# Kernel optimization log

Measured on AMD Instinct MI355X. Metric: run time of the kernel, lower is better.

## Reference

```python
import jax, jax.numpy as jnp
import numpy as np

H_IMG, W_IMG = 64, 64          # token grid (n = H*W = 4096)
D_MODEL = 512
N_HEADS = 8
D1 = 1024                      # expand_ratio * d_model, multiple of n_heads
HEAD_DIM = D1 // N_HEADS       # 128
RANK = 32
NK = 16                        # inducing points for SKI interpolation


def interp_weights(n, nk):
    # inverse-time warp: position i -> 1/(i+1) in (0,1], linearly interpolated
    # onto nk uniform inducing points in [0,1] (2 nonzeros per row).
    pos = 1.0 / (jnp.arange(n, dtype=jnp.float32) + 1.0)
    t = pos * (nk - 1)
    idx = jnp.clip(jnp.floor(t).astype(jnp.int32), 0, nk - 2)
    frac = t - idx.astype(jnp.float32)
    r = jnp.arange(n)
    Wm = jnp.zeros((n, nk), jnp.float32)
    Wm = Wm.at[r, idx].set(1.0 - frac).at[r, idx + 1].set(frac)
    return Wm  # (n, nk)


def apply_toep(v, U, V):
    # v: (b, m, n, h, d); low-rank SKI Toeplitz mixing along axis n.
    # T ~= (Wm @ U) (Wm @ V)^T per head  -> O(n*r*d) instead of O(n^2*d).
    n = v.shape[2]
    nk = U.shape[1]
    Wm = interp_weights(n, nk)                      # (n, nk)
    A = jnp.einsum('nk,hkr->hnr', Wm, U)            # (h, n, r)
    B = jnp.einsum('nk,hkr->hnr', Wm, V)            # (h, n, r)
    tmp = jnp.einsum('hnr,bmnhd->bmhrd', B, v)      # contract over n
    return jnp.einsum('hnr,bmhrd->bmnhd', A, tmp)


def setup_inputs() -> dict:
    key = jax.random.key(0)
    ks = jax.random.split(key, 12)
    s = 0.02
    x = jax.random.normal(ks[0], (16, H_IMG * W_IMG, D_MODEL), jnp.float32)
    Wu = s * jax.random.normal(ks[1], (D1, D_MODEL), jnp.float32)
    bu = s * jax.random.normal(ks[2], (D1,), jnp.float32)
    Wv = s * jax.random.normal(ks[3], (D1, D_MODEL), jnp.float32)
    bv = s * jax.random.normal(ks[4], (D1,), jnp.float32)
    Wo = s * jax.random.normal(ks[5], (D_MODEL, D1), jnp.float32)
    bo = s * jax.random.normal(ks[6], (D_MODEL,), jnp.float32)
    U1 = s * jax.random.normal(ks[7], (N_HEADS, NK, RANK), jnp.float32)
    V1 = s * jax.random.normal(ks[8], (N_HEADS, NK, RANK), jnp.float32)
    U2 = s * jax.random.normal(ks[9], (N_HEADS, NK, RANK), jnp.float32)
    V2 = s * jax.random.normal(ks[10], (N_HEADS, NK, RANK), jnp.float32)
    return {'x': x, 'Wu': Wu, 'bu': bu, 'Wv': Wv, 'bv': bv, 'Wo': Wo,
            'bo': bo, 'U1': U1, 'V1': V1, 'U2': U2, 'V2': V2}


def reference(x, Wu, bu, Wv, bv, Wo, bo, U1, V1, U2, V2):
    b, n, _ = x.shape
    H = int(np.sqrt(n)); W = n // H
    u = jax.nn.silu(x @ Wu.T + bu)                  # (b, n, d1)
    v = jax.nn.silu(x @ Wv.T + bv)                  # (b, n, d1)
    v4 = v.reshape(b, H, W, N_HEADS, HEAD_DIM)      # (b, H, W, h, d)

    # o1: toep1 along W, then toep2 along H
    t = apply_toep(v4, U1, V1)                      # mix along W
    t = t.transpose(0, 2, 1, 3, 4)                  # (b, W, H, h, d)
    t = apply_toep(t, U2, V2)                       # mix along H
    o1 = t.transpose(0, 2, 1, 3, 4)

    # o2: toep2 along H, then toep1 along W
    s_ = v4.transpose(0, 2, 1, 3, 4)                # (b, W, H, h, d)
    s_ = apply_toep(s_, U2, V2)                     # mix along H
    s_ = s_.transpose(0, 2, 1, 3, 4)                # (b, H, W, h, d)
    o2 = apply_toep(s_, U1, V1)                     # mix along W

    out = (o1 + o2).reshape(b, n, D1)
    out = u * out                                   # gated token mixing
    return out @ Wo.T + bo                          # (b, n, d_model)
```

## Files before the change

kernel.cpp:

```cpp
#include <hip/hip_runtime.h>
#include <hip/hip_bf16.h>

typedef unsigned short u16;
typedef unsigned int   u32;
typedef float  f32x4  __attribute__((ext_vector_type(4)));
typedef __bf16 bf16x8 __attribute__((ext_vector_type(8)));
typedef u16    u16x8  __attribute__((ext_vector_type(8)));
typedef u16    u16x4  __attribute__((ext_vector_type(4)));

__device__ __forceinline__ u16 f2bf(float f) {
  u32 x = __builtin_bit_cast(u32, f);
  x += 0x7fffu + ((x >> 16) & 1u);
  return (u16)(x >> 16);
}
__device__ __forceinline__ float bf2f(u16 u) {
  return __builtin_bit_cast(float, (u32)u << 16);
}
__device__ __forceinline__ void gload_lds16(const u16* g, u16* l) {
  __builtin_amdgcn_global_load_lds(
      (const __attribute__((address_space(1))) void*)g,
      (__attribute__((address_space(3))) void*)l, 16, 0, 0);
}

__global__ void k_conv_x(const float* __restrict__ x, u16* __restrict__ xb) {
  int g = blockIdx.x * 256 + threadIdx.x;
  const float4* src = (const float4*)(x + (size_t)g * 8);
  float4 f0 = src[0], f1 = src[1];
  u16x8 o;
  o[0]=f2bf(f0.x); o[1]=f2bf(f0.y); o[2]=f2bf(f0.z); o[3]=f2bf(f0.w);
  o[4]=f2bf(f1.x); o[5]=f2bf(f1.y); o[6]=f2bf(f1.z); o[7]=f2bf(f1.w);
  *(u16x8*)(xb + (size_t)g * 8) = o;
}

__global__ void k_conv_w(const float* __restrict__ Wu, const float* __restrict__ Wv,
                         const float* __restrict__ Wo, const float* __restrict__ bu,
                         const float* __restrict__ bv, u16* __restrict__ wuvb,
                         u16* __restrict__ wob, float* __restrict__ biasuv) {
  int g = blockIdx.x * 256 + threadIdx.x;
  int e = g * 4;
  const float* src; u16* dst;
  if (e < 524288)        { src = Wu + e;             dst = wuvb + e; }
  else if (e < 1048576)  { src = Wv + (e - 524288);  dst = wuvb + e; }
  else                   { src = Wo + (e - 1048576); dst = wob + (e - 1048576); }
  float4 f = *(const float4*)src;
  u16x4 o; o[0]=f2bf(f.x); o[1]=f2bf(f.y); o[2]=f2bf(f.z); o[3]=f2bf(f.w);
  *(u16x4*)dst = o;
  if (g < 2048) biasuv[g] = (g < 1024) ? bu[g] : bv[g - 1024];
}

__global__ void k_toep(const float* __restrict__ U1, const float* __restrict__ V1,
                       const float* __restrict__ U2, const float* __restrict__ V2,
                       u16* __restrict__ T1b, u16* __restrict__ T2b) {
  __shared__ float Us[512], Vs[512];
  int bid = blockIdx.x, t = threadIdx.x;
  int which = bid >> 6, rest = bid & 63, h = rest >> 3, seg = rest & 7;
  const float* U = which ? U2 : U1;
  const float* V = which ? V2 : V1;
  u16* T = which ? T2b : T1b;
  float scale = which ? 2.0f : 1.0f;
  for (int i = t; i < 512; i += 256) { Us[i] = U[h*512 + i]; Vs[i] = V[h*512 + i]; }
  __syncthreads();
  for (int q = 0; q < 2; ++q) {
    int e = seg * 512 + q * 256 + t;
    int i = e >> 6, j = e & 63;
    float pi = 1.0f / (float)(i + 1); float tvi = pi * 15.0f;
    int ii = min((int)floorf(tvi), 14); float fi = tvi - (float)ii;
    float pj = 1.0f / (float)(j + 1); float tvj = pj * 15.0f;
    int jj = min((int)floorf(tvj), 14); float fj = tvj - (float)jj;
    float s = 0.0f;
    #pragma unroll
    for (int r = 0; r < 32; ++r) {
      float a = (1.0f - fi) * Us[ii*32 + r] + fi * Us[(ii+1)*32 + r];
      float b = (1.0f - fj) * Vs[jj*32 + r] + fj * Vs[(jj+1)*32 + r];
      s += a * b;
    }
    T[h*4096 + i*64 + j] = f2bf(s * scale);
  }
}

template<int EPI>
__global__ __launch_bounds__(512, 2) void k_gemm256(
    const u16* __restrict__ A, const u16* __restrict__ B,
    const float* __restrict__ bias, void* __restrict__ C,
    int K, int nbn, int ldc) {
  extern __shared__ uint4 smem4[];
  u16* lds = (u16*)smem4;
  const int t = threadIdx.x;
  const int l = t & 63, w = t >> 6;
  const int wmi = w >> 2, wni = w & 3;
  const int nwg = gridDim.x;
  const int lb = (blockIdx.x & 7) * (nwg >> 3) + (blockIdx.x >> 3);
  const int bm = lb / nbn, bn = lb % nbn;
  const u16* Ab = A + (size_t)bm * 256 * K;
  const u16* Bb = B + (size_t)bn * 256 * K;
  const int NT = K >> 6;

  f32x4 acc[8][4];
  #pragma unroll
  for (int i = 0; i < 8; ++i)
    #pragma unroll
    for (int j = 0; j < 4; ++j) acc[i][j] = (f32x4){0.f, 0.f, 0.f, 0.f};

#define STAGE(gop) do {                                                      \
    int _g = (gop);                                                          \
    int _tile = _g >> 2, _half = _g & 3;                                     \
    int _kt = _tile << 6;                                                    \
    const u16* _src = (_half < 2) ? Ab : Bb;                                 \
    int _rowbase = (_half & 1) << 7;                                         \
    u16* _dst = lds + (_tile & 1) * 32768 + ((_half >= 2) ? 16384 : 0)       \
                + _rowbase * 64;                                             \
    _Pragma("unroll")                                                        \
    for (int _j = 0; _j < 2; ++_j) {                                         \
      int _idx = _j * 512 + t;                                               \
      int _rr = _idx >> 3, _s8 = _idx & 7;                                   \
      int _R = _rowbase + _rr;                                               \
      int _col = (_s8 ^ (_R & 7)) << 3;                                      \
      gload_lds16(_src + (size_t)_R * K + _kt + _col, _dst + _idx * 8);      \
    }                                                                        \
  } while (0)

#define READ_A(hh, fp) do {                                                  \
    _Pragma("unroll")                                                        \
    for (int ks = 0; ks < 2; ++ks)                                           \
      _Pragma("unroll")                                                      \
      for (int i = 0; i < 2; ++i) {                                          \
        int R = ((hh) << 7) + (wmi << 6) + ((fp) * 2 + i) * 16 + (l & 15);   \
        int q8 = ks * 4 + (l >> 4);                                          \
        af[ks*2+i] = *(const bf16x8*)&As[R * 64 + ((q8 ^ (R & 7)) << 3)];    \
      }                                                                      \
  } while (0)

#define MFMA_PHASE(hh, fp) do {                                              \
    __builtin_amdgcn_s_setprio(1);                                           \
    _Pragma("unroll")                                                        \
    for (int ks = 0; ks < 2; ++ks)                                           \
      _Pragma("unroll")                                                      \
      for (int i = 0; i < 2; ++i)                                            \
        _Pragma("unroll")                                                    \
        for (int nf = 0; nf < 4; ++nf)                                       \
          acc[(hh)*4+(fp)*2+i][nf] = __builtin_amdgcn_mfma_f32_16x16x32_bf16(\
              af[ks*2+i], bfv[ks*4+nf], acc[(hh)*4+(fp)*2+i][nf], 0, 0, 0);  \
    __builtin_amdgcn_s_setprio(0);                                           \
  } while (0)

  STAGE(0); STAGE(1); STAGE(2); STAGE(3);
  STAGE(6); STAGE(7); STAGE(4);
  asm volatile("s_waitcnt vmcnt(6)");
  __builtin_amdgcn_s_barrier();

  for (int tile = 0; tile < NT; ++tile) {
    const u16* As = lds + (tile & 1) * 32768;
    const u16* Bs = As + 16384;
    bf16x8 bfv[8];
    bf16x8 af[4];

    #pragma unroll
    for (int ks = 0; ks < 2; ++ks)
      #pragma unroll
      for (int nf = 0; nf < 4; ++nf) {
        int R = (wni << 6) + nf * 16 + (l & 15);
        int q8 = ks * 4 + (l >> 4);
        bfv[ks*4+nf] = *(const bf16x8*)&Bs[R * 64 + ((q8 ^ (R & 7)) << 3)];
      }
    READ_A(0, 0);
    if (tile + 1 < NT) STAGE(4 * (tile + 1) + 1);
    __builtin_amdgcn_s_barrier();
    asm volatile("s_waitcnt lgkmcnt(0)");
    MFMA_PHASE(0, 0);
    __builtin_amdgcn_s_barrier();

    READ_A(0, 1);
    if (tile + 2 < NT) { STAGE(4*(tile+2)+2); STAGE(4*(tile+2)+3); }
    __builtin_amdgcn_s_barrier();
    asm volatile("s_waitcnt lgkmcnt(0)");
    MFMA_PHASE(0, 1);
    if (tile < NT - 2)       asm volatile("s_waitcnt vmcnt(12)");
    else if (tile == NT - 2) asm volatile("s_waitcnt vmcnt(8)");
    else                     asm volatile("s_waitcnt vmcnt(0)");
    __builtin_amdgcn_s_barrier();

    READ_A(1, 0);
    if (tile + 2 < NT) STAGE(4 * (tile + 2) + 0);
    __builtin_amdgcn_s_barrier();
    asm volatile("s_waitcnt lgkmcnt(0)");
    MFMA_PHASE(1, 0);
    __builtin_amdgcn_s_barrier();

    READ_A(1, 1);
    __builtin_amdgcn_s_barrier();
    asm volatile("s_waitcnt lgkmcnt(0)");
    MFMA_PHASE(1, 1);
    if (tile < NT - 2)       asm volatile("s_waitcnt vmcnt(8)");
    else if (tile == NT - 2) asm volatile("s_waitcnt vmcnt(2)");
    __builtin_amdgcn_s_barrier();
  }
#undef STAGE
#undef READ_A
#undef MFMA_PHASE

  float bcol[4];
  #pragma unroll
  for (int nf = 0; nf < 4; ++nf)
    bcol[nf] = bias[bn * 256 + (wni << 6) + nf * 16 + (l & 15)];
  #pragma unroll
  for (int hf = 0; hf < 8; ++hf) {
    int gm0 = bm * 256 + (hf >> 2) * 128 + wmi * 64 + (hf & 3) * 16 + (l >> 4) * 4;
    #pragma unroll
    for (int nf = 0; nf < 4; ++nf) {
      int gn = bn * 256 + (wni << 6) + nf * 16 + (l & 15);
      #pragma unroll
      for (int r = 0; r < 4; ++r) {
        float z = acc[hf][nf][r] + bcol[nf];
        size_t off = (size_t)(gm0 + r) * ldc + gn;
        if (EPI == 0) {
          z = z / (1.0f + __expf(-z));
          ((u16*)C)[off] = f2bf(z);
        } else {
          ((float*)C)[off] = z;
        }
      }
    }
  }
}

template<int PASS>
__global__ __launch_bounds__(256) void k_mix(const u16* __restrict__ uv,
                                             u16* __restrict__ y,
                                             const u16* __restrict__ Tmat) {
  __shared__ alignas(16) u16 Ts[64 * 72];
  __shared__ alignas(16) u32 VT[128 * 36];
  int bid = blockIdx.x, t = threadIdx.x;
  int h = bid & 7, outer = (bid >> 3) & 63, b = bid >> 9;
  int l = t & 63, w = t >> 6;

  {
    const u16* Tg = Tmat + h * 4096;
    int rr = t >> 2, cc = (t & 3) * 16;
    const uint4* src = (const uint4*)(Tg + rr * 64 + cc);
    uint4 v0 = src[0], v1 = src[1];
    *(uint4*)&Ts[rr * 72 + cc] = v0;
    *(uint4*)&Ts[rr * 72 + cc + 8] = v1;
  }

  size_t inbase; size_t instride;
  if (PASS == 0) { inbase = ((size_t)(b*64 + outer) * 64) * 2048 + 1024 + h*128; instride = 2048; }
  else           { inbase = ((size_t)b * 4096 + outer) * 1024 + h*128;            instride = 65536; }
  const u16* inp = (PASS == 0) ? uv : (const u16*)y;

  #pragma unroll
  for (int a2 = 0; a2 < 2; ++a2) {
    int jp = (t >> 4) + a2 * 16;
    int dc = t & 15;
    const u16* r0 = inp + inbase + (size_t)(2*jp) * instride + dc * 8;
    const u16* r1 = r0 + instride;
    uint4 av = *(const uint4*)r0;
    uint4 bv = *(const uint4*)r1;
    u32 a4[4] = {av.x, av.y, av.z, av.w};
    u32 b4[4] = {bv.x, bv.y, bv.z, bv.w};
    #pragma unroll
    for (int ww = 0; ww < 4; ++ww) {
      u32 lo = (a4[ww] & 0xffffu) | (b4[ww] << 16);
      u32 hi = (a4[ww] >> 16) | (b4[ww] & 0xffff0000u);
      int d0 = dc * 8 + 2 * ww, d1 = d0 + 1;
      VT[d0 * 36 + (jp ^ ((((u32)d0 >> 3) & 7) << 2))] = lo;
      VT[d1 * 36 + (jp ^ ((((u32)d1 >> 3) & 7) << 2))] = hi;
    }
  }
  __syncthreads();

  f32x4 acc[8];
  #pragma unroll
  for (int nf = 0; nf < 8; ++nf) acc[nf] = (f32x4){0.f, 0.f, 0.f, 0.f};
  #pragma unroll
  for (int ks = 0; ks < 2; ++ks) {
    bf16x8 af = *(const bf16x8*)&Ts[(w*16 + (l & 15)) * 72 + ks*32 + (l >> 4)*8];
    #pragma unroll
    for (int nf = 0; nf < 8; ++nf) {
      int d  = nf * 16 + (l & 15);
      int kd = ks * 16 + (l >> 4) * 4;
      u32 dw = (u32)d * 36 + ((u32)kd ^ ((((u32)d >> 3) & 7) << 2));
      bf16x8 bfv = *(const bf16x8*)&VT[dw];
      acc[nf] = __builtin_amdgcn_mfma_f32_16x16x32_bf16(af, bfv, acc[nf], 0, 0, 0);
    }
  }

  size_t obase, ostride, ubase = 0;
  if (PASS == 0) { obase = ((size_t)(b*64 + outer) * 64) * 1024 + h*128; ostride = 1024; }
  else {
    obase = ((size_t)b * 4096 + outer) * 1024 + h*128; ostride = 65536;
    ubase = ((size_t)b * 4096 + outer) * 2048 + h*128;
  }
  #pragma unroll
  for (int nf = 0; nf < 8; ++nf) {
    int d = nf * 16 + (l & 15);
    #pragma unroll
    for (int r = 0; r < 4; ++r) {
      int m = w * 16 + (l >> 4) * 4 + r;
      float val = acc[nf][r];
      if (PASS == 1) val *= bf2f(uv[ubase + (size_t)m * 131072 + d]);
      y[obase + (size_t)m * ostride + d] = f2bf(val);
    }
  }
}

extern "C" void kernel_launch(void* const* d_in, const int* in_sizes, int n_in,
                              void* d_out, int out_size, void* d_ws, size_t ws_size,
                              hipStream_t stream) {
  const float* x  = (const float*)d_in[0];
  const float* Wu = (const float*)d_in[1];
  const float* bu = (const float*)d_in[2];
  const float* Wv = (const float*)d_in[3];
  const float* bv = (const float*)d_in[4];
  const float* Wo = (const float*)d_in[5];
  const float* bo = (const float*)d_in[6];
  const float* U1 = (const float*)d_in[7];
  const float* V1 = (const float*)d_in[8];
  const float* U2 = (const float*)d_in[9];
  const float* V2 = (const float*)d_in[10];
  float* out = (float*)d_out;

  char* p = (char*)d_ws;
  u16*  xb     = (u16*)(p + 0);
  u16*  wuvb   = (u16*)(p + 67108864);
  u16*  wob    = (u16*)(p + 69206016);
  u16*  T1b    = (u16*)(p + 70254592);
  u16*  T2b    = (u16*)(p + 70320128);
  float* biasuv= (float*)(p + 70385664);
  u16*  uv     = (u16*)(p + 70393856);
  u16*  y      = (u16*)(p + 338829312);
  if (ws_size < 473047040ULL) return;

  (void)hipFuncSetAttribute((const void*)&k_gemm256<0>,
      hipFuncAttributeMaxDynamicSharedMemorySize, 131072);
  (void)hipFuncSetAttribute((const void*)&k_gemm256<1>,
      hipFuncAttributeMaxDynamicSharedMemorySize, 131072);

  k_conv_x<<<16384, 256, 0, stream>>>(x, xb);
  k_conv_w<<<1536, 256, 0, stream>>>(Wu, Wv, Wo, bu, bv, wuvb, wob, biasuv);
  k_toep<<<128, 256, 0, stream>>>(U1, V1, U2, V2, T1b, T2b);
  k_gemm256<0><<<2048, 512, 131072, stream>>>(xb, wuvb, biasuv, (void*)uv, 512, 8, 2048);
  k_mix<0><<<8192, 256, 0, stream>>>(uv, y, T1b);
  k_mix<1><<<8192, 256, 0, stream>>>(uv, y, T2b);
  k_gemm256<1><<<512, 512, 131072, stream>>>(y, wob, bo, (void*)out, 1024, 2, 512);
}
```

Baseline: 516.8 us.

## Make GEMMs persistent over multiple M tiles with continuous cross-tile prefetch

Both GEMM kernels now launch 256 workgroups, each looping over several 256x256 output tiles along M (8 for the up-projection, 2 for the output projection). The tile loop is one long pipeline, so prefetch of the next tile's K slices overlaps the epilogue of the current one, and the bias is loaded once per workgroup. K, the tile count and the leading dimension become template constants. This aims to remove per-workgroup launch, prologue and drain costs and pipeline bubbles, at the cost of fixed tiling assumptions and in-loop epilogue register pressure.

After: 519.1 us (median of 4 runs). About the same (+0.4%).

```diff
diff --git a/kernel.cpp b/kernel.cpp
--- a/kernel.cpp
+++ b/kernel.cpp
@@ -78,22 +78,25 @@
   }
 }
 
-template<int EPI>
+template<int EPI, int K, int NSEQ, int LGNBN, int LDC>
 __global__ __launch_bounds__(512, 2) void k_gemm256(
     const u16* __restrict__ A, const u16* __restrict__ B,
-    const float* __restrict__ bias, void* __restrict__ C,
-    int K, int nbn, int ldc) {
+    const float* __restrict__ bias, void* __restrict__ C) {
+  constexpr int NT = K >> 6;
+  constexpr int LGNT = (NT == 8) ? 3 : 4;
+  constexpr int TOT = NSEQ * NT;
+  constexpr int SMSTEP = 256 / NSEQ;
+  constexpr size_t SEQA = (size_t)SMSTEP * 256 * K;
   extern __shared__ uint4 smem4[];
   u16* lds = (u16*)smem4;
   const int t = threadIdx.x;
   const int l = t & 63, w = t >> 6;
   const int wmi = w >> 2, wni = w & 3;
-  const int nwg = gridDim.x;
-  const int lb = (blockIdx.x & 7) * (nwg >> 3) + (blockIdx.x >> 3);
-  const int bm = lb / nbn, bn = lb % nbn;
-  const u16* Ab = A + (size_t)bm * 256 * K;
+  const int e = (blockIdx.x & 7) * 32 + (blockIdx.x >> 3);
+  const int bn = e & ((1 << LGNBN) - 1);
+  const int bm0 = e >> LGNBN;
+  const u16* Ab = A + (size_t)bm0 * 256 * K;
   const u16* Bb = B + (size_t)bn * 256 * K;
-  const int NT = K >> 6;
 
   f32x4 acc[8][4];
   #pragma unroll
@@ -101,13 +104,18 @@
     #pragma unroll
     for (int j = 0; j < 4; ++j) acc[i][j] = (f32x4){0.f, 0.f, 0.f, 0.f};
 
-#define STAGE(gop) do {                                                      \
-    int _g = (gop);                                                          \
-    int _tile = _g >> 2, _half = _g & 3;                                     \
-    int _kt = _tile << 6;                                                    \
-    const u16* _src = (_half < 2) ? Ab : Bb;                                 \
-    int _rowbase = (_half & 1) << 7;                                         \
-    u16* _dst = lds + (_tile & 1) * 32768 + ((_half >= 2) ? 16384 : 0)       \
+  float bcol[4];
+  #pragma unroll
+  for (int nf = 0; nf < 4; ++nf)
+    bcol[nf] = bias[bn * 256 + (wni << 6) + nf * 16 + (l & 15)];
+
+#define STAGE(TILE, HALF) do {                                               \
+    int _t = (TILE);                                                         \
+    int _seq = _t >> LGNT;                                                   \
+    size_t _kt = (size_t)((_t & (NT - 1)) << 6);                             \
+    const u16* _src = ((HALF) < 2) ? (Ab + (size_t)_seq * SEQA) : Bb;        \
+    constexpr int _rowbase = ((HALF) & 1) << 7;                              \
+    u16* _dst = lds + (_t & 1) * 32768 + (((HALF) >= 2) ? 16384 : 0)         \
                 + _rowbase * 64;                                             \
     _Pragma("unroll")                                                        \
     for (int _j = 0; _j < 2; ++_j) {                                         \
@@ -143,12 +151,12 @@
     __builtin_amdgcn_s_setprio(0);                                           \
   } while (0)
 
-  STAGE(0); STAGE(1); STAGE(2); STAGE(3);
-  STAGE(6); STAGE(7); STAGE(4);
+  STAGE(0, 0); STAGE(0, 1); STAGE(0, 2); STAGE(0, 3);
+  STAGE(1, 2); STAGE(1, 3); STAGE(1, 0);
   asm volatile("s_waitcnt vmcnt(6)");
   __builtin_amdgcn_s_barrier();
 
-  for (int tile = 0; tile < NT; ++tile) {
+  for (int tile = 0; tile < TOT; ++tile) {
     const u16* As = lds + (tile & 1) * 32768;
     const u16* Bs = As + 16384;
     bf16x8 bfv[8];
@@ -163,24 +171,24 @@
         bfv[ks*4+nf] = *(const bf16x8*)&Bs[R * 64 + ((q8 ^ (R & 7)) << 3)];
       }
     READ_A(0, 0);
-    if (tile + 1 < NT) STAGE(4 * (tile + 1) + 1);
+    if (tile + 1 < TOT) STAGE(tile + 1, 1);
     __builtin_amdgcn_s_barrier();
     asm volatile("s_waitcnt lgkmcnt(0)");
     MFMA_PHASE(0, 0);
     __builtin_amdgcn_s_barrier();
 
     READ_A(0, 1);
-    if (tile + 2 < NT) { STAGE(4*(tile+2)+2); STAGE(4*(tile+2)+3); }
+    if (tile + 2 < TOT) { STAGE(tile + 2, 2); STAGE(tile + 2, 3); }
     __builtin_amdgcn_s_barrier();
     asm volatile("s_waitcnt lgkmcnt(0)");
     MFMA_PHASE(0, 1);
-    if (tile < NT - 2)       asm volatile("s_waitcnt vmcnt(12)");
-    else if (tile == NT - 2) asm volatile("s_waitcnt vmcnt(8)");
-    else                     asm volatile("s_waitcnt vmcnt(0)");
+    if (tile < TOT - 2)       asm volatile("s_waitcnt vmcnt(12)");
+    else if (tile == TOT - 2) asm volatile("s_waitcnt vmcnt(8)");
+    else                      asm volatile("s_waitcnt vmcnt(0)");
     __builtin_amdgcn_s_barrier();
 
     READ_A(1, 0);
-    if (tile + 2 < NT) STAGE(4 * (tile + 2) + 0);
+    if (tile + 2 < TOT) STAGE(tile + 2, 0);
     __builtin_amdgcn_s_barrier();
     asm volatile("s_waitcnt lgkmcnt(0)");
     MFMA_PHASE(1, 0);
@@ -190,37 +198,41 @@
     __builtin_amdgcn_s_barrier();
     asm volatile("s_waitcnt lgkmcnt(0)");
     MFMA_PHASE(1, 1);
-    if (tile < NT - 2)       asm volatile("s_waitcnt vmcnt(8)");
-    else if (tile == NT - 2) asm volatile("s_waitcnt vmcnt(2)");
-    __builtin_amdgcn_s_barrier();
+    if (tile < TOT - 2)       asm volatile("s_waitcnt vmcnt(8)");
+    else if (tile == TOT - 2) asm volatile("s_waitcnt vmcnt(2)");
+    __builtin_amdgcn_s_barrier();
+
+    if ((tile & (NT - 1)) == NT - 1) {
+      int s = tile >> LGNT;
+      int bmbase = (bm0 + s * SMSTEP) * 256;
+      #pragma unroll
+      for (int hf = 0; hf < 8; ++hf) {
+        int gm0 = bmbase + (hf >> 2) * 128 + wmi * 64 + (hf & 3) * 16 + (l >> 4) * 4;
+        #pragma unroll
+        for (int nf = 0; nf < 4; ++nf) {
+          int gn = bn * 256 + (wni << 6) + nf * 16 + (l & 15);
+          #pragma unroll
+          for (int r = 0; r < 4; ++r) {
+            float z = acc[hf][nf][r] + bcol[nf];
+            size_t off = (size_t)(gm0 + r) * LDC + gn;
+            if (EPI == 0) {
+              z = z / (1.0f + __expf(-z));
+              ((u16*)C)[off] = f2bf(z);
+            } else {
+              ((float*)C)[off] = z;
+            }
+          }
+        }
+      }
+      #pragma unroll
+      for (int i = 0; i < 8; ++i)
+        #pragma unroll
+        for (int j = 0; j < 4; ++j) acc[i][j] = (f32x4){0.f, 0.f, 0.f, 0.f};
+    }
   }
 #undef STAGE
 #undef READ_A
 #undef MFMA_PHASE
-
-  float bcol[4];
-  #pragma unroll
-  for (int nf = 0; nf < 4; ++nf)
-    bcol[nf] = bias[bn * 256 + (wni << 6) + nf * 16 + (l & 15)];
-  #pragma unroll
-  for (int hf = 0; hf < 8; ++hf) {
-    int gm0 = bm * 256 + (hf >> 2) * 128 + wmi * 64 + (hf & 3) * 16 + (l >> 4) * 4;
-    #pragma unroll
-    for (int nf = 0; nf < 4; ++nf) {
-      int gn = bn * 256 + (wni << 6) + nf * 16 + (l & 15);
-      #pragma unroll
-      for (int r = 0; r < 4; ++r) {
-        float z = acc[hf][nf][r] + bcol[nf];
-        size_t off = (size_t)(gm0 + r) * ldc + gn;
-        if (EPI == 0) {
-          z = z / (1.0f + __expf(-z));
-          ((u16*)C)[off] = f2bf(z);
-        } else {
-          ((float*)C)[off] = z;
-        }
-      }
-    }
-  }
 }
 
 template<int PASS>
@@ -330,16 +342,16 @@
   u16*  y      = (u16*)(p + 338829312);
   if (ws_size < 473047040ULL) return;
 
-  (void)hipFuncSetAttribute((const void*)&k_gemm256<0>,
+  (void)hipFuncSetAttribute((const void*)&k_gemm256<0, 512, 8, 3, 2048>,
       hipFuncAttributeMaxDynamicSharedMemorySize, 131072);
-  (void)hipFuncSetAttribute((const void*)&k_gemm256<1>,
+  (void)hipFuncSetAttribute((const void*)&k_gemm256<1, 1024, 2, 1, 512>,
       hipFuncAttributeMaxDynamicSharedMemorySize, 131072);
 
   k_conv_x<<<16384, 256, 0, stream>>>(x, xb);
   k_conv_w<<<1536, 256, 0, stream>>>(Wu, Wv, Wo, bu, bv, wuvb, wob, biasuv);
   k_toep<<<128, 256, 0, stream>>>(U1, V1, U2, V2, T1b, T2b);
-  k_gemm256<0><<<2048, 512, 131072, stream>>>(xb, wuvb, biasuv, (void*)uv, 512, 8, 2048);
+  k_gemm256<0, 512, 8, 3, 2048><<<256, 512, 131072, stream>>>(xb, wuvb, biasuv, (void*)uv);
   k_mix<0><<<8192, 256, 0, stream>>>(uv, y, T1b);
   k_mix<1><<<8192, 256, 0, stream>>>(uv, y, T2b);
-  k_gemm256<1><<<512, 512, 131072, stream>>>(y, wob, bo, (void*)out, 1024, 2, 512);
-}
+  k_gemm256<1, 1024, 2, 1, 512><<<256, 512, 131072, stream>>>(y, wob, bo, (void*)out);
+}
```
